# Performance work log

Hardware: AMD Instinct MI355X
Metric: run time of the kernel (lower is better)

Reference implementation:

```python
import jax, jax.numpy as jnp
import numpy as np

N = 8192
IN_DIM = 256
OUT_DIM = 256
NEG_INF = -9e15


def setup_inputs() -> dict:
    key = jax.random.key(0)
    k1, k2, k3, k4, k5 = jax.random.split(key, 5)
    worker_x = jax.random.normal(k1, (N, IN_DIM), dtype=jnp.float32)
    ww_adj = jax.random.randint(k2, (N, N), 0, 2, dtype=jnp.int32)
    # learned params (xavier-ish scales)
    W = jax.random.normal(k3, (IN_DIM, OUT_DIM), dtype=jnp.float32) * (1.0 / np.sqrt(IN_DIM))
    a_src = jax.random.normal(k4, (OUT_DIM, 1), dtype=jnp.float32) * (1.414 / np.sqrt(OUT_DIM))
    a_dst = jax.random.normal(k5, (OUT_DIM, 1), dtype=jnp.float32) * (1.414 / np.sqrt(OUT_DIM))
    return {"worker_x": worker_x, "ww_adj": ww_adj, "W": W, "a_src": a_src, "a_dst": a_dst}


def reference(worker_x, ww_adj, W, a_src, a_dst):
    Wh = worker_x @ W                       # [N, out_dim]
    f_src = Wh @ a_src                      # [N, 1]
    f_dst = Wh @ a_dst                      # [N, 1]
    e = jax.nn.leaky_relu(f_src + f_dst.T, negative_slope=0.2)  # [N, N]
    attention = jnp.where(ww_adj > 0, e, NEG_INF)
    attention = jax.nn.softmax(attention, axis=-1)
    h_prime = attention @ Wh                # [N, out_dim]
    return jax.nn.elu(h_prime)
```

## Files before the change

kernel.cpp:

```cpp
#include <hip/hip_runtime.h>
#include <stdint.h>

typedef __attribute__((ext_vector_type(8))) short short8;
typedef __attribute__((ext_vector_type(4))) float f32x4;
typedef __attribute__((ext_vector_type(4))) _Float16 h16x4;

#define LOG2E 1.4426950408889634f

#define OFF_WTT   0u
#define OFF_WHTB  131072u
#define OFF_BITS  4325376u
#define OFF_FSRC  12713984u
#define OFF_FDST  12746752u
#define OFF_MKEY  12779520u
#define OFF_LP    12779584u
#define OFF_ACCH  12910656u

__device__ __forceinline__ unsigned short f2bf(float f) {
    union { float f; unsigned int i; } v; v.f = f;
    unsigned int u = v.i;
    return (unsigned short)((u + 0x7FFFu + ((u >> 16) & 1u)) >> 16);
}

__global__ void k0_init(const float* __restrict__ W,
                        unsigned short* __restrict__ WTt,
                        unsigned int* __restrict__ Mkey) {
    int idx = blockIdx.x * 256 + threadIdx.x;
    int i = idx >> 8, o = idx & 255;
    WTt[(i >> 5) * 8192 + ((i >> 3) & 3) * 2048 + o * 8 + (i & 7)] = f2bf(W[idx]);
    if (idx == 0) *Mkey = 0u;
}

__global__ __launch_bounds__(256, 8)
void k_pack(const int* __restrict__ adj, unsigned long long* __restrict__ bits64) {
    int wave_id = (blockIdx.x * 256 + threadIdx.x) >> 6;
    int lane = threadIdx.x & 63;
    const int* p = adj + (size_t)wave_id * 16384 + lane;
    unsigned long long* bp = bits64 + (size_t)wave_id * 256;
    for (int it = 0; it < 256; it += 8) {
        int v[8];
#pragma unroll
        for (int u = 0; u < 8; ++u) v[u] = p[(size_t)(it + u) * 64];
#pragma unroll
        for (int u = 0; u < 8; ++u) {
            unsigned long long m = __ballot(v[u] > 0);
            if (lane == 0) bp[it + u] = m;
        }
    }
}

__global__ __launch_bounds__(256, 2)
void k1_stage1(const float* __restrict__ X,
               const unsigned short* __restrict__ WTt,
               const float* __restrict__ a_src,
               const float* __restrict__ a_dst,
               unsigned short* __restrict__ WhTb,
               float* __restrict__ f_src,
               float* __restrict__ f_dst,
               unsigned int* __restrict__ Mkey) {
    __shared__ __align__(16) unsigned short Bt[8192];
    __shared__ float fsum[64];
    const int t = threadIdx.x, w = t >> 6, lane = t & 63, l15 = lane & 15, q = lane >> 4;
    const int rg = w & 1, cg = w >> 1;
    const int i0 = blockIdx.x * 32;
    const int arow = i0 + rg * 16 + l15;

    if (t < 64) fsum[t] = 0.f;

    float as[8], ad[8];
#pragma unroll
    for (int ci = 0; ci < 8; ++ci) {
        int col = cg * 128 + ci * 16 + l15;
        as[ci] = a_src[col]; ad[ci] = a_dst[col];
    }

    f32x4 acc[8];
#pragma unroll
    for (int ci = 0; ci < 8; ++ci) acc[ci] = (f32x4)0.f;

    for (int ks = 0; ks < 8; ++ks) {
        __syncthreads();
        {
            const uint4* src = (const uint4*)(WTt + ks * 8192);
            uint4* dst = (uint4*)Bt;
            dst[t] = src[t]; dst[256 + t] = src[256 + t];
            dst[512 + t] = src[512 + t]; dst[768 + t] = src[768 + t];
        }
        __syncthreads();
        const float* xp = X + (size_t)arow * 256 + ks * 32 + q * 8;
        float4 xa = *(const float4*)xp;
        float4 xb = *(const float4*)(xp + 4);
        short8 a;
        a[0] = (short)f2bf(xa.x); a[1] = (short)f2bf(xa.y);
        a[2] = (short)f2bf(xa.z); a[3] = (short)f2bf(xa.w);
        a[4] = (short)f2bf(xb.x); a[5] = (short)f2bf(xb.y);
        a[6] = (short)f2bf(xb.z); a[7] = (short)f2bf(xb.w);
#pragma unroll
        for (int ci = 0; ci < 8; ++ci) {
            short8 b = *(const short8*)((const char*)Bt + q * 4096 + (cg * 128 + ci * 16 + l15) * 16);
            acc[ci] = __builtin_amdgcn_mfma_f32_16x16x32_bf16(a, b, acc[ci], 0, 0, 0);
        }
    }

#pragma unroll
    for (int ci = 0; ci < 8; ++ci) {
        int col = cg * 128 + ci * 16 + l15;
        ushort4 v;
        v.x = f2bf(acc[ci][0]); v.y = f2bf(acc[ci][1]);
        v.z = f2bf(acc[ci][2]); v.w = f2bf(acc[ci][3]);
        size_t flat = (size_t)(i0 >> 5) * 8192 + (size_t)(rg * 2 + (q >> 1)) * 2048
                      + (size_t)col * 8 + (q & 1) * 4;
        *(ushort4*)(WhTb + flat) = v;
    }

#pragma unroll
    for (int reg = 0; reg < 4; ++reg) {
        float ps = 0.f, pd = 0.f;
#pragma unroll
        for (int ci = 0; ci < 8; ++ci) {
            ps += acc[ci][reg] * as[ci];
            pd += acc[ci][reg] * ad[ci];
        }
#pragma unroll
        for (int m = 1; m < 16; m <<= 1) {
            ps += __shfl_xor(ps, m, 64);
            pd += __shfl_xor(pd, m, 64);
        }
        if (l15 == 0) {
            atomicAdd(&fsum[rg * 16 + q * 4 + reg], ps);
            atomicAdd(&fsum[32 + rg * 16 + q * 4 + reg], pd);
        }
    }
    __syncthreads();
    if (t < 32) {
        int row = i0 + t;
        float ps = fsum[t], pd = fsum[32 + t];
        f_src[row] = ps;
        f_dst[row] = pd;
        union { float f; unsigned int u; } cv; cv.f = pd;
        unsigned int key = (cv.u & 0x80000000u) ? ~cv.u : (cv.u | 0x80000000u);
        atomicMax(Mkey, key);
    }
}

__global__ __launch_bounds__(256, 4)
void k2_flash(const unsigned int* __restrict__ BITS,
              const unsigned short* __restrict__ WhTb,
              const float* __restrict__ f_src,
              const float* __restrict__ f_dst,
              const unsigned int* __restrict__ Mkey,
              float* __restrict__ Lp,
              _Float16* __restrict__ ACCh) {
    __shared__ __align__(16) unsigned short Bt[2][8192];
    __shared__ float fd_s[2048];
    const int t = threadIdx.x, w = t >> 6, lane = t & 63, l15 = lane & 15, q = lane >> 4;
    const int i0 = blockIdx.x * 64;
    const int jc = blockIdx.y;
    const int jb0 = jc * 2048, jw0 = jc * 64;
    const int rA = i0 + w * 16 + l15;

    unsigned int key = *Mkey;
    union { unsigned int u; float f; } mv;
    mv.u = (key & 0x80000000u) ? (key & 0x7FFFFFFFu) : ~key;
    const float Mf = mv.f;
    const float fsA = f_src[rA];
    float vA = fsA + Mf; const float mcA = fmaxf(vA, 0.2f * vA) * LOG2E;

    {
        float4* d = (float4*)fd_s;
        const float4* src = (const float4*)(f_dst + jb0);
        d[t] = src[t]; d[256 + t] = src[256 + t];
    }
    {
        const uint4* src = (const uint4*)(WhTb + (size_t)jw0 * 8192);
        uint4* dst = (uint4*)&Bt[0][0];
        dst[t] = src[t]; dst[256 + t] = src[256 + t];
        dst[512 + t] = src[512 + t]; dst[768 + t] = src[768 + t];
    }
    const unsigned int* bpA = BITS + (size_t)rA * 256 + jw0;
    unsigned int pwA = bpA[0];

    f32x4 acc[16];
#pragma unroll
    for (int ci = 0; ci < 16; ++ci) acc[ci] = (f32x4)0.f;
    float lsA = 0.f;
    __syncthreads();

    for (int js = 0; js < 64; ++js) {
        const int buf = js & 1;
        const int jn = (js + 1) & 63;
        const uint4* nsrc = (const uint4*)(WhTb + (size_t)(jw0 + jn) * 8192);
        uint4 g0 = nsrc[t], g1 = nsrc[256 + t], g2 = nsrc[512 + t], g3 = nsrc[768 + t];
        unsigned int nwA = bpA[jn];

        const float* fdp = fd_s + js * 32 + q * 8;
        float4 f0 = *(const float4*)fdp, f1 = *(const float4*)(fdp + 4);
        float fdv[8] = { f0.x, f0.y, f0.z, f0.w, f1.x, f1.y, f1.z, f1.w };

        unsigned int bA = pwA >> (q * 8);
        short8 fragA;
#pragma unroll
        for (int k = 0; k < 8; ++k) {
            float tA = fsA + fdv[k];
            float eA = fmaxf(tA, 0.2f * tA);
            float pA = __builtin_amdgcn_exp2f(__builtin_fmaf(eA, LOG2E, -mcA));
            pA = ((bA >> k) & 1u) ? pA : 0.f;
            lsA += pA; fragA[k] = (short)f2bf(pA);
        }

        const char* base = (const char*)&Bt[buf][0] + q * 4096 + l15 * 16;
#pragma unroll
        for (int ci = 0; ci < 16; ++ci) {
            short8 bf = *(const short8*)(base + ci * 256);
            acc[ci] = __builtin_amdgcn_mfma_f32_16x16x32_bf16(fragA, bf, acc[ci], 0, 0, 0);
        }

        { uint4* dst = (uint4*)&Bt[buf ^ 1][0];
          dst[t] = g0; dst[256 + t] = g1; dst[512 + t] = g2; dst[768 + t] = g3; }
        pwA = nwA;
        __syncthreads();
    }

    lsA += __shfl_xor(lsA, 16, 64); lsA += __shfl_xor(lsA, 32, 64);
    if (lane < 16) Lp[(size_t)jc * 8192 + i0 + w * 16 + lane] = lsA;

    _Float16* ap = ACCh + (size_t)jc * 2097152;
#pragma unroll
    for (int ci = 0; ci < 16; ++ci) {
#pragma unroll
        for (int reg = 0; reg < 4; ++reg) {
            int row = i0 + w * 16 + q * 4 + reg;
            ap[(size_t)row * 256 + ci * 16 + l15] = (_Float16)acc[ci][reg];
        }
    }
}

__global__ void k4_final(const _Float16* __restrict__ ACCh,
                         const float* __restrict__ Lp,
                         float* __restrict__ out) {
    int gid = blockIdx.x * 256 + threadIdx.x;
    int i = gid >> 6;
    float s0 = 0.f, s1 = 0.f, s2 = 0.f, s3 = 0.f;
#pragma unroll
    for (int jc = 0; jc < 4; ++jc) {
        h16x4 v = *(const h16x4*)(ACCh + (size_t)jc * 2097152 + (size_t)gid * 4);
        s0 += (float)v[0]; s1 += (float)v[1]; s2 += (float)v[2]; s3 += (float)v[3];
    }
    float L = 0.f;
#pragma unroll
    for (int jc = 0; jc < 4; ++jc) L += Lp[jc * 8192 + i];
    float inv = (L > 0.f) ? (1.0f / L) : 0.f;
    float h0 = s0 * inv, h1 = s1 * inv, h2 = s2 * inv, h3 = s3 * inv;
    float4 o;
    o.x = (h0 > 0.f) ? h0 : expm1f(h0);
    o.y = (h1 > 0.f) ? h1 : expm1f(h1);
    o.z = (h2 > 0.f) ? h2 : expm1f(h2);
    o.w = (h3 > 0.f) ? h3 : expm1f(h3);
    *(float4*)(out + (size_t)gid * 4) = o;
}

extern "C" void kernel_launch(void* const* d_in, const int* in_sizes, int n_in,
                              void* d_out, int out_size, void* d_ws, size_t ws_size,
                              hipStream_t stream) {
    (void)in_sizes; (void)n_in; (void)out_size; (void)ws_size;
    const float* X   = (const float*)d_in[0];
    const int*   adj = (const int*)d_in[1];
    const float* W   = (const float*)d_in[2];
    const float* a_s = (const float*)d_in[3];
    const float* a_d = (const float*)d_in[4];

    char* ws = (char*)d_ws;
    unsigned short* WTt  = (unsigned short*)(ws + OFF_WTT);
    unsigned short* WhTb = (unsigned short*)(ws + OFF_WHTB);
    unsigned long long* B64 = (unsigned long long*)(ws + OFF_BITS);
    unsigned int*   BITS = (unsigned int*)(ws + OFF_BITS);
    float*          fsrc = (float*)(ws + OFF_FSRC);
    float*          fdst = (float*)(ws + OFF_FDST);
    unsigned int*   Mkey = (unsigned int*)(ws + OFF_MKEY);
    float*          Lp   = (float*)(ws + OFF_LP);
    _Float16*       ACCh = (_Float16*)(ws + OFF_ACCH);
    float*          out  = (float*)d_out;

    k0_init<<<dim3(256), dim3(256), 0, stream>>>(W, WTt, Mkey);
    k_pack<<<dim3(1024), dim3(256), 0, stream>>>(adj, B64);
    k1_stage1<<<dim3(256), dim3(256), 0, stream>>>(X, WTt, a_s, a_d, WhTb, fsrc, fdst, Mkey);
    k2_flash<<<dim3(128, 4), dim3(256), 0, stream>>>(BITS, WhTb, fsrc, fdst, Mkey, Lp, ACCh);
    k4_final<<<dim3(2048), dim3(256), 0, stream>>>(ACCh, Lp, out);
}
```

Measured before the change: 459.4 us.

## Restructure flash kernel: 128-row tiles, 8-way j split, direct global B loads

The attention-times-Wh kernel now gives each wave two 16-row blocks that share the same B fragments, doubling reuse of every loaded Wh tile. B is read straight from global memory (L2) instead of being double-buffered through LDS with a barrier each step, and the adjacency bit words are preloaded into padded shared memory. The j dimension is split eight ways instead of four to keep enough blocks, so the final reduction kernel and the ACCh workspace grow. The trade-off is higher register pressure (launch bounds drop to 2), more global load latency exposed in the MFMA loop, and more partial-sum traffic.

```diff
diff --git a/kernel.cpp b/kernel.cpp
--- a/kernel.cpp
+++ b/kernel.cpp
@@ -14,7 +14,7 @@
 #define OFF_FDST  12746752u
 #define OFF_MKEY  12779520u
 #define OFF_LP    12779584u
-#define OFF_ACCH  12910656u
+#define OFF_ACCH  13041728u
 
 __device__ __forceinline__ unsigned short f2bf(float f) {
     union { float f; unsigned int i; } v; v.f = f;
@@ -143,7 +143,7 @@
     }
 }
 
-__global__ __launch_bounds__(256, 4)
+__global__ __launch_bounds__(256, 2)
 void k2_flash(const unsigned int* __restrict__ BITS,
               const unsigned short* __restrict__ WhTb,
               const float* __restrict__ f_src,
@@ -151,54 +151,49 @@
               const unsigned int* __restrict__ Mkey,
               float* __restrict__ Lp,
               _Float16* __restrict__ ACCh) {
-    __shared__ __align__(16) unsigned short Bt[2][8192];
-    __shared__ float fd_s[2048];
+    __shared__ float fd_s[1024];
+    __shared__ unsigned int bits_s[128 * 33];
     const int t = threadIdx.x, w = t >> 6, lane = t & 63, l15 = lane & 15, q = lane >> 4;
-    const int i0 = blockIdx.x * 64;
+    const int i0 = blockIdx.x * 128;
     const int jc = blockIdx.y;
-    const int jb0 = jc * 2048, jw0 = jc * 64;
-    const int rA = i0 + w * 16 + l15;
+    const int jb0 = jc * 1024;
+    const int jw0 = jc * 32;
+
+    { float4* d = (float4*)fd_s; d[t] = ((const float4*)(f_dst + jb0))[t]; }
+#pragma unroll
+    for (int s = 0; s < 16; ++s) {
+        int idx = s * 256 + t;
+        int row = idx >> 5, word = idx & 31;
+        bits_s[row * 33 + word] = BITS[(size_t)(i0 + row) * 256 + jw0 + word];
+    }
 
     unsigned int key = *Mkey;
     union { unsigned int u; float f; } mv;
     mv.u = (key & 0x80000000u) ? (key & 0x7FFFFFFFu) : ~key;
     const float Mf = mv.f;
-    const float fsA = f_src[rA];
+    const int rA = i0 + w * 32 + l15;
+    const float fsA = f_src[rA], fsB = f_src[rA + 16];
     float vA = fsA + Mf; const float mcA = fmaxf(vA, 0.2f * vA) * LOG2E;
-
-    {
-        float4* d = (float4*)fd_s;
-        const float4* src = (const float4*)(f_dst + jb0);
-        d[t] = src[t]; d[256 + t] = src[256 + t];
-    }
-    {
-        const uint4* src = (const uint4*)(WhTb + (size_t)jw0 * 8192);
-        uint4* dst = (uint4*)&Bt[0][0];
-        dst[t] = src[t]; dst[256 + t] = src[256 + t];
-        dst[512 + t] = src[512 + t]; dst[768 + t] = src[768 + t];
-    }
-    const unsigned int* bpA = BITS + (size_t)rA * 256 + jw0;
-    unsigned int pwA = bpA[0];
-
-    f32x4 acc[16];
-#pragma unroll
-    for (int ci = 0; ci < 16; ++ci) acc[ci] = (f32x4)0.f;
-    float lsA = 0.f;
+    float vB = fsB + Mf; const float mcB = fmaxf(vB, 0.2f * vB) * LOG2E;
     __syncthreads();
 
-    for (int js = 0; js < 64; ++js) {
-        const int buf = js & 1;
-        const int jn = (js + 1) & 63;
-        const uint4* nsrc = (const uint4*)(WhTb + (size_t)(jw0 + jn) * 8192);
-        uint4 g0 = nsrc[t], g1 = nsrc[256 + t], g2 = nsrc[512 + t], g3 = nsrc[768 + t];
-        unsigned int nwA = bpA[jn];
-
+    const unsigned short* Bbase = WhTb + (size_t)jw0 * 8192 + q * 2048 + l15 * 8;
+    const unsigned int* brA = &bits_s[(w * 32 + l15) * 33];
+    const unsigned int* brB = &bits_s[(w * 32 + 16 + l15) * 33];
+
+    f32x4 accA[16], accB[16];
+#pragma unroll
+    for (int ci = 0; ci < 16; ++ci) { accA[ci] = (f32x4)0.f; accB[ci] = (f32x4)0.f; }
+    float lsA = 0.f, lsB = 0.f;
+
+    for (int js = 0; js < 32; ++js) {
         const float* fdp = fd_s + js * 32 + q * 8;
         float4 f0 = *(const float4*)fdp, f1 = *(const float4*)(fdp + 4);
         float fdv[8] = { f0.x, f0.y, f0.z, f0.w, f1.x, f1.y, f1.z, f1.w };
-
-        unsigned int bA = pwA >> (q * 8);
-        short8 fragA;
+        unsigned int bA = brA[js] >> (q * 8);
+        unsigned int bB = brB[js] >> (q * 8);
+
+        short8 fragA, fragB;
 #pragma unroll
         for (int k = 0; k < 8; ++k) {
             float tA = fsA + fdv[k];
@@ -206,31 +201,46 @@
             float pA = __builtin_amdgcn_exp2f(__builtin_fmaf(eA, LOG2E, -mcA));
             pA = ((bA >> k) & 1u) ? pA : 0.f;
             lsA += pA; fragA[k] = (short)f2bf(pA);
-        }
-
-        const char* base = (const char*)&Bt[buf][0] + q * 4096 + l15 * 16;
-#pragma unroll
-        for (int ci = 0; ci < 16; ++ci) {
-            short8 bf = *(const short8*)(base + ci * 256);
-            acc[ci] = __builtin_amdgcn_mfma_f32_16x16x32_bf16(fragA, bf, acc[ci], 0, 0, 0);
-        }
-
-        { uint4* dst = (uint4*)&Bt[buf ^ 1][0];
-          dst[t] = g0; dst[256 + t] = g1; dst[512 + t] = g2; dst[768 + t] = g3; }
-        pwA = nwA;
-        __syncthreads();
+            float tB = fsB + fdv[k];
+            float eB = fmaxf(tB, 0.2f * tB);
+            float pB = __builtin_amdgcn_exp2f(__builtin_fmaf(eB, LOG2E, -mcB));
+            pB = ((bB >> k) & 1u) ? pB : 0.f;
+            lsB += pB; fragB[k] = (short)f2bf(pB);
+        }
+
+        const unsigned short* bp = Bbase + (size_t)js * 8192;
+        short8 bf[8];
+#pragma unroll
+        for (int ci = 0; ci < 8; ++ci) bf[ci] = *(const short8*)(bp + ci * 128);
+#pragma unroll
+        for (int ci = 0; ci < 8; ++ci) {
+            accA[ci] = __builtin_amdgcn_mfma_f32_16x16x32_bf16(fragA, bf[ci], accA[ci], 0, 0, 0);
+            accB[ci] = __builtin_amdgcn_mfma_f32_16x16x32_bf16(fragB, bf[ci], accB[ci], 0, 0, 0);
+        }
+#pragma unroll
+        for (int ci = 0; ci < 8; ++ci) bf[ci] = *(const short8*)(bp + (ci + 8) * 128);
+#pragma unroll
+        for (int ci = 0; ci < 8; ++ci) {
+            accA[8 + ci] = __builtin_amdgcn_mfma_f32_16x16x32_bf16(fragA, bf[ci], accA[8 + ci], 0, 0, 0);
+            accB[8 + ci] = __builtin_amdgcn_mfma_f32_16x16x32_bf16(fragB, bf[ci], accB[8 + ci], 0, 0, 0);
+        }
     }
 
     lsA += __shfl_xor(lsA, 16, 64); lsA += __shfl_xor(lsA, 32, 64);
-    if (lane < 16) Lp[(size_t)jc * 8192 + i0 + w * 16 + lane] = lsA;
+    lsB += __shfl_xor(lsB, 16, 64); lsB += __shfl_xor(lsB, 32, 64);
+    if (lane < 16) {
+        Lp[(size_t)jc * 8192 + i0 + w * 32 + lane] = lsA;
+        Lp[(size_t)jc * 8192 + i0 + w * 32 + 16 + lane] = lsB;
+    }
 
     _Float16* ap = ACCh + (size_t)jc * 2097152;
 #pragma unroll
     for (int ci = 0; ci < 16; ++ci) {
 #pragma unroll
         for (int reg = 0; reg < 4; ++reg) {
-            int row = i0 + w * 16 + q * 4 + reg;
-            ap[(size_t)row * 256 + ci * 16 + l15] = (_Float16)acc[ci][reg];
+            int rowA = i0 + w * 32 + q * 4 + reg;
+            ap[(size_t)rowA * 256 + ci * 16 + l15] = (_Float16)accA[ci][reg];
+            ap[(size_t)(rowA + 16) * 256 + ci * 16 + l15] = (_Float16)accB[ci][reg];
         }
     }
 }
@@ -242,13 +252,13 @@
     int i = gid >> 6;
     float s0 = 0.f, s1 = 0.f, s2 = 0.f, s3 = 0.f;
 #pragma unroll
-    for (int jc = 0; jc < 4; ++jc) {
+    for (int jc = 0; jc < 8; ++jc) {
         h16x4 v = *(const h16x4*)(ACCh + (size_t)jc * 2097152 + (size_t)gid * 4);
         s0 += (float)v[0]; s1 += (float)v[1]; s2 += (float)v[2]; s3 += (float)v[3];
     }
     float L = 0.f;
 #pragma unroll
-    for (int jc = 0; jc < 4; ++jc) L += Lp[jc * 8192 + i];
+    for (int jc = 0; jc < 8; ++jc) L += Lp[jc * 8192 + i];
     float inv = (L > 0.f) ? (1.0f / L) : 0.f;
     float h0 = s0 * inv, h1 = s1 * inv, h2 = s2 * inv, h3 = s3 * inv;
     float4 o;
@@ -284,6 +294,6 @@
     k0_init<<<dim3(256), dim3(256), 0, stream>>>(W, WTt, Mkey);
     k_pack<<<dim3(1024), dim3(256), 0, stream>>>(adj, B64);
     k1_stage1<<<dim3(256), dim3(256), 0, stream>>>(X, WTt, a_s, a_d, WhTb, fsrc, fdst, Mkey);
-    k2_flash<<<dim3(128, 4), dim3(256), 0, stream>>>(BITS, WhTb, fsrc, fdst, Mkey, Lp, ACCh);
+    k2_flash<<<dim3(64, 8), dim3(256), 0, stream>>>(BITS, WhTb, fsrc, fdst, Mkey, Lp, ACCh);
     k4_final<<<dim3(2048), dim3(256), 0, stream>>>(ACCh, Lp, out);
 }
```

Result: slower. 485.5 us (+5.7%).

## Fuse adjacency bit-packing into flash kernel with async LDS staging

Applied to the files above, without the earlier changes.

Removes the separate pack kernel. Each flash block now ballots its own 64x2048 adjacency tile into a shared-memory bitmask before the main loop, so the packed bit array no longer has to be written to and read back from global memory. The block grows to 512 threads, with pairs of waves splitting the 256 output columns. WhTb tiles are staged straight into LDS with global_load_lds instead of going through registers. The adjacency load now runs as a serial prologue that is not overlapped with the MFMA loop. It also adds LDS pressure, and correctness depends on the async LDS loads completing before the barrier.

```diff
diff --git a/kernel.cpp b/kernel.cpp
--- a/kernel.cpp
+++ b/kernel.cpp
@@ -9,7 +9,6 @@
 
 #define OFF_WTT   0u
 #define OFF_WHTB  131072u
-#define OFF_BITS  4325376u
 #define OFF_FSRC  12713984u
 #define OFF_FDST  12746752u
 #define OFF_MKEY  12779520u
@@ -20,6 +19,13 @@
     union { float f; unsigned int i; } v; v.f = f;
     unsigned int u = v.i;
     return (unsigned short)((u + 0x7FFFu + ((u >> 16) & 1u)) >> 16);
+}
+
+__device__ __forceinline__ void stage16(const unsigned short* g, unsigned short* l) {
+    __builtin_amdgcn_global_load_lds(
+        (const __attribute__((address_space(1))) unsigned int*)g,
+        (__attribute__((address_space(3))) unsigned int*)l,
+        16, 0, 0);
 }
 
 __global__ void k0_init(const float* __restrict__ W,
@@ -29,24 +35,6 @@
     int i = idx >> 8, o = idx & 255;
     WTt[(i >> 5) * 8192 + ((i >> 3) & 3) * 2048 + o * 8 + (i & 7)] = f2bf(W[idx]);
     if (idx == 0) *Mkey = 0u;
-}
-
-__global__ __launch_bounds__(256, 8)
-void k_pack(const int* __restrict__ adj, unsigned long long* __restrict__ bits64) {
-    int wave_id = (blockIdx.x * 256 + threadIdx.x) >> 6;
-    int lane = threadIdx.x & 63;
-    const int* p = adj + (size_t)wave_id * 16384 + lane;
-    unsigned long long* bp = bits64 + (size_t)wave_id * 256;
-    for (int it = 0; it < 256; it += 8) {
-        int v[8];
-#pragma unroll
-        for (int u = 0; u < 8; ++u) v[u] = p[(size_t)(it + u) * 64];
-#pragma unroll
-        for (int u = 0; u < 8; ++u) {
-            unsigned long long m = __ballot(v[u] > 0);
-            if (lane == 0) bp[it + u] = m;
-        }
-    }
 }
 
 __global__ __launch_bounds__(256, 2)
@@ -143,8 +131,8 @@
     }
 }
 
-__global__ __launch_bounds__(256, 4)
-void k2_flash(const unsigned int* __restrict__ BITS,
+__global__ __launch_bounds__(512, 4)
+void k2_fused(const int* __restrict__ adj,
               const unsigned short* __restrict__ WhTb,
               const float* __restrict__ f_src,
               const float* __restrict__ f_dst,
@@ -152,52 +140,74 @@
               float* __restrict__ Lp,
               _Float16* __restrict__ ACCh) {
     __shared__ __align__(16) unsigned short Bt[2][8192];
+    __shared__ unsigned int bits_s[64 * 65];
     __shared__ float fd_s[2048];
     const int t = threadIdx.x, w = t >> 6, lane = t & 63, l15 = lane & 15, q = lane >> 4;
+    const int rg = w >> 1, cg = w & 1;
     const int i0 = blockIdx.x * 64;
     const int jc = blockIdx.y;
-    const int jb0 = jc * 2048, jw0 = jc * 64;
-    const int rA = i0 + w * 16 + l15;
+    const int jb0 = jc * 2048;
+    const int jw0 = jc * 64;
 
     unsigned int key = *Mkey;
     union { unsigned int u; float f; } mv;
     mv.u = (key & 0x80000000u) ? (key & 0x7FFFFFFFu) : ~key;
     const float Mf = mv.f;
+    const int rA = i0 + rg * 16 + l15;
     const float fsA = f_src[rA];
     float vA = fsA + Mf; const float mcA = fmaxf(vA, 0.2f * vA) * LOG2E;
 
+    { float4* d = (float4*)fd_s; d[t] = ((const float4*)(f_dst + jb0))[t]; }
+
     {
-        float4* d = (float4*)fd_s;
-        const float4* src = (const float4*)(f_dst + jb0);
-        d[t] = src[t]; d[256 + t] = src[256 + t];
-    }
-    {
-        const uint4* src = (const uint4*)(WhTb + (size_t)jw0 * 8192);
-        uint4* dst = (uint4*)&Bt[0][0];
-        dst[t] = src[t]; dst[256 + t] = src[256 + t];
-        dst[512 + t] = src[512 + t]; dst[768 + t] = src[768 + t];
-    }
-    const unsigned int* bpA = BITS + (size_t)rA * 256 + jw0;
-    unsigned int pwA = bpA[0];
-
-    f32x4 acc[16];
-#pragma unroll
-    for (int ci = 0; ci < 16; ++ci) acc[ci] = (f32x4)0.f;
+        const unsigned short* gsrc = WhTb + (size_t)jw0 * 8192;
+#pragma unroll
+        for (int s = 0; s < 2; ++s)
+            stage16(gsrc + s * 4096 + t * 8,
+                    (unsigned short*)((char*)&Bt[0][0] + s * 8192 + w * 1024));
+    }
+
+    for (int g = 0; g < 32; ++g) {
+        int v[8];
+#pragma unroll
+        for (int u = 0; u < 8; ++u) {
+            int idx = g * 8 + u, r = idx >> 5, c = idx & 31;
+            v[u] = adj[(size_t)(i0 + w * 8 + r) * 8192 + jb0 + c * 64 + lane];
+        }
+#pragma unroll
+        for (int u = 0; u < 8; ++u) {
+            int idx = g * 8 + u, r = idx >> 5, c = idx & 31;
+            unsigned long long m = __ballot(v[u] > 0);
+            if (lane == 0) {
+                bits_s[(w * 8 + r) * 65 + 2 * c]     = (unsigned int)m;
+                bits_s[(w * 8 + r) * 65 + 2 * c + 1] = (unsigned int)(m >> 32);
+            }
+        }
+    }
+
+    f32x4 acc[8];
+#pragma unroll
+    for (int ci = 0; ci < 8; ++ci) acc[ci] = (f32x4)0.f;
     float lsA = 0.f;
     __syncthreads();
 
     for (int js = 0; js < 64; ++js) {
         const int buf = js & 1;
         const int jn = (js + 1) & 63;
-        const uint4* nsrc = (const uint4*)(WhTb + (size_t)(jw0 + jn) * 8192);
-        uint4 g0 = nsrc[t], g1 = nsrc[256 + t], g2 = nsrc[512 + t], g3 = nsrc[768 + t];
-        unsigned int nwA = bpA[jn];
-
+
+        {
+            const unsigned short* gsrc = WhTb + (size_t)(jw0 + jn) * 8192;
+#pragma unroll
+            for (int s = 0; s < 2; ++s)
+                stage16(gsrc + s * 4096 + t * 8,
+                        (unsigned short*)((char*)&Bt[buf ^ 1][0] + s * 8192 + w * 1024));
+        }
+
+        unsigned int word = bits_s[(rg * 16 + l15) * 65 + js];
+        unsigned int bA = word >> (q * 8);
         const float* fdp = fd_s + js * 32 + q * 8;
         float4 f0 = *(const float4*)fdp, f1 = *(const float4*)(fdp + 4);
         float fdv[8] = { f0.x, f0.y, f0.z, f0.w, f1.x, f1.y, f1.z, f1.w };
-
-        unsigned int bA = pwA >> (q * 8);
         short8 fragA;
 #pragma unroll
         for (int k = 0; k < 8; ++k) {
@@ -208,29 +218,27 @@
             lsA += pA; fragA[k] = (short)f2bf(pA);
         }
 
-        const char* base = (const char*)&Bt[buf][0] + q * 4096 + l15 * 16;
-#pragma unroll
-        for (int ci = 0; ci < 16; ++ci) {
+        const char* base = (const char*)&Bt[buf][0] + q * 4096 + (cg * 128 + l15) * 16;
+#pragma unroll
+        for (int ci = 0; ci < 8; ++ci) {
             short8 bf = *(const short8*)(base + ci * 256);
             acc[ci] = __builtin_amdgcn_mfma_f32_16x16x32_bf16(fragA, bf, acc[ci], 0, 0, 0);
         }
 
-        { uint4* dst = (uint4*)&Bt[buf ^ 1][0];
-          dst[t] = g0; dst[256 + t] = g1; dst[512 + t] = g2; dst[768 + t] = g3; }
-        pwA = nwA;
         __syncthreads();
     }
 
     lsA += __shfl_xor(lsA, 16, 64); lsA += __shfl_xor(lsA, 32, 64);
-    if (lane < 16) Lp[(size_t)jc * 8192 + i0 + w * 16 + lane] = lsA;
+    if (cg == 0 && lane < 16)
+        Lp[(size_t)jc * 8192 + i0 + rg * 16 + lane] = lsA;
 
     _Float16* ap = ACCh + (size_t)jc * 2097152;
 #pragma unroll
-    for (int ci = 0; ci < 16; ++ci) {
+    for (int ci = 0; ci < 8; ++ci) {
 #pragma unroll
         for (int reg = 0; reg < 4; ++reg) {
-            int row = i0 + w * 16 + q * 4 + reg;
-            ap[(size_t)row * 256 + ci * 16 + l15] = (_Float16)acc[ci][reg];
+            int row = i0 + rg * 16 + q * 4 + reg;
+            ap[(size_t)row * 256 + cg * 128 + ci * 16 + l15] = (_Float16)acc[ci][reg];
         }
     }
 }
@@ -272,8 +280,6 @@
     char* ws = (char*)d_ws;
     unsigned short* WTt  = (unsigned short*)(ws + OFF_WTT);
     unsigned short* WhTb = (unsigned short*)(ws + OFF_WHTB);
-    unsigned long long* B64 = (unsigned long long*)(ws + OFF_BITS);
-    unsigned int*   BITS = (unsigned int*)(ws + OFF_BITS);
     float*          fsrc = (float*)(ws + OFF_FSRC);
     float*          fdst = (float*)(ws + OFF_FDST);
     unsigned int*   Mkey = (unsigned int*)(ws + OFF_MKEY);
@@ -282,8 +288,7 @@
     float*          out  = (float*)d_out;
 
     k0_init<<<dim3(256), dim3(256), 0, stream>>>(W, WTt, Mkey);
-    k_pack<<<dim3(1024), dim3(256), 0, stream>>>(adj, B64);
     k1_stage1<<<dim3(256), dim3(256), 0, stream>>>(X, WTt, a_s, a_d, WhTb, fsrc, fdst, Mkey);
-    k2_flash<<<dim3(128, 4), dim3(256), 0, stream>>>(BITS, WhTb, fsrc, fdst, Mkey, Lp, ACCh);
+    k2_fused<<<dim3(128, 4), dim3(512), 0, stream>>>(adj, WhTb, fsrc, fdst, Mkey, Lp, ACCh);
     k4_final<<<dim3(2048), dim3(256), 0, stream>>>(ACCh, Lp, out);
 }
```

Measured after the change: 467.5 us. No clear change (+1.8%).
